# Kernel optimization log

Measured on AMD Instinct MI355X. Metric: run time of the kernel, lower is better.

## Reference

```python
import jax, jax.numpy as jnp
import numpy as np

THETA = 1.0  # integrate-and-fire threshold


def conv2d_t(x, w, b, padding):
    # x: [N,C,H,W,T]; torch snn.conv is Conv3d with kernel (k,k,1) => per-timestep 2D conv
    N, C, H, W, T = x.shape
    xt = jnp.moveaxis(x, -1, 1).reshape(N * T, C, H, W)
    y = jax.lax.conv_general_dilated(
        xt, w, (1, 1), [(padding, padding), (padding, padding)],
        dimension_numbers=('NCHW', 'OIHW', 'NCHW'))
    y = y + b[None, :, None, None]
    O, Ho, Wo = y.shape[1:]
    return jnp.moveaxis(y.reshape(N, T, O, Ho, Wo), 1, -1)


def avg_pool2_t(x):
    # snn.pool(2): fixed-weight 2x2 conv == 2x2 average pool, applied per timestep
    N, C, H, W, T = x.shape
    return x.reshape(N, C, H // 2, 2, W // 2, 2, T).mean(axis=(3, 5))


def dense_t(x, w, b):
    # snn.dense: Conv3d over full spatial extent == linear over flattened C*H*W, per timestep
    N = x.shape[0]; T = x.shape[-1]
    xf = x.reshape(N, -1, T)  # flatten in (C,H,W) order, matching torch conv3d weight layout
    return jnp.einsum('nft,of->not', xf, w) + b[None, :, None]


def spike(x):
    # Temporal LIF (integrate-and-fire, soft reset) scanned over trailing time dim.
    def step(u, xt):
        u = u + xt
        s = (u >= THETA).astype(x.dtype)
        u = u - s * THETA
        return u, s
    xt = jnp.moveaxis(x, -1, 0)  # [T, ...]
    _, s = jax.lax.scan(step, jnp.zeros(x.shape[:-1], x.dtype), xt)
    return jnp.moveaxis(s, 0, -1)


def setup_inputs() -> dict:
    key = jax.random.key(0)
    ks = jax.random.split(key, 20)
    f32 = jnp.float32
    def w(k, shape, fan_in):
        return jax.random.normal(k, shape, f32) * np.float32(1.0 / np.sqrt(fan_in))
    inp = {
        'x':  jax.random.uniform(ks[0], (128, 1, 28, 28, 16), f32),
        'w1': w(ks[1], (32, 1, 3, 3), 9),      'b1': jnp.zeros((32,), f32),
        'w2': w(ks[2], (32, 32, 3, 3), 288),   'b2': jnp.zeros((32,), f32),
        'w3': w(ks[3], (32, 32, 3, 3), 288),   'b3': jnp.zeros((32,), f32),
        'w4': w(ks[4], (16, 32, 1, 1), 32),    'b4': jnp.zeros((16,), f32),
        'w5': w(ks[5], (16, 16, 3, 3), 144),   'b5': jnp.zeros((16,), f32),
        'w6': w(ks[6], (32, 16, 1, 1), 16),    'b6': jnp.zeros((32,), f32),
        'wf1': w(ks[7], (128, 32 * 14 * 14), 32 * 14 * 14), 'bf1': jnp.zeros((128,), f32),
        'wf2': w(ks[8], (10, 128), 128),       'bf2': jnp.zeros((10,), f32),
    }
    return inp


def reference(x, w1, b1, w2, b2, w3, b3, w4, b4, w5, b5, w6, b6, wf1, bf1, wf2, bf2):
    T = x.shape[-1]
    h = spike(conv2d_t(x, w1, b1, 1))
    y = h
    h = spike(conv2d_t(h, w2, b2, 1))
    h = spike(conv2d_t(h, w3, b3, 1) + y)
    h = spike(avg_pool2_t(h))
    y1 = h
    h = spike(conv2d_t(h, w4, b4, 0))
    h = spike(conv2d_t(h, w5, b5, 1))
    h = spike(conv2d_t(h, w6, b6, 0) + y1)
    h = spike(dense_t(h, wf1, bf1))
    h = spike(dense_t(h, wf2, bf2))
    return h.sum(axis=-1) / T  # [N, 10] firing rates
```

## Files before the change

kernel.cpp:

```cpp
#include <hip/hip_runtime.h>

typedef unsigned short u16;
typedef unsigned int u32;
typedef unsigned long long u64;
typedef __attribute__((ext_vector_type(4))) int i32x4;
typedef __attribute__((ext_vector_type(16))) int i32x16;

#define TT 16
#define Z16 {0, 0, 0, 0, 0, 0, 0, 0, 0, 0, 0, 0, 0, 0, 0, 0}

__device__ __forceinline__ u32 scan_spike(const double* acc) {
  double u = 0.0;
  u32 m = 0;
#pragma unroll
  for (int t = 0; t < TT; ++t) {
    u += acc[t];
    if (u >= 1.0) { m |= (1u << t); u -= 1.0; }
  }
  return m;
}

__device__ __forceinline__ long long shfl_xor64(long long v, int m) {
  int lo = __shfl_xor((int)(v & 0xffffffffLL), m);
  int hi = __shfl_xor((int)(v >> 32), m);
  return ((long long)hi << 32) | (u32)lo;
}

__device__ __forceinline__ float conv1_fetch(const float* __restrict__ xn,
                                             int y0, int r, int col, int t) {
  int yi = y0 - 1 + r, xi = col - 1;
  if ((unsigned)yi < 28u && (unsigned)xi < 28u)
    return xn[((size_t)(yi * 28 + xi)) * 16 + t];
  return 0.0f;
}

__global__ __launch_bounds__(448) void conv1_lds(
    const float* __restrict__ x, const float* __restrict__ w,
    const float* __restrict__ b, u16* __restrict__ out) {
  __shared__ float xt[2][4][30][20];
  __shared__ float wl[32][9];

  int blk = blockIdx.x;
  int n = blk >> 1;
  int half = blk & 1;
  int ypBase = half * 7;
  int tid = threadIdx.x;

  for (int i = tid; i < 288; i += 448) wl[i / 9][i % 9] = w[i];

  int sr_[5], sc_[5], st_[5];
  bool sok[5];
#pragma unroll
  for (int k = 0; k < 5; ++k) {
    int i = tid + k * 448;
    sok[k] = (i < 1920);
    int ii = sok[k] ? i : 0;
    sr_[k] = ii / 480;
    int rem = ii % 480;
    sc_[k] = rem / 16;
    st_[k] = rem % 16;
  }
  const float* xn = x + (size_t)n * (28 * 28 * 16);

  int ocg = tid & 7;
  int xx = (tid >> 3) % 28;
  int dy = tid / 224;
  int oc0 = ocg * 4;

  {
    int y0 = ypBase * 2;
#pragma unroll
    for (int k = 0; k < 5; ++k)
      if (sok[k])
        xt[0][sr_[k]][sc_[k]][st_[k]] =
            conv1_fetch(xn, y0, sr_[k], sc_[k], st_[k]);
  }
  __syncthreads();

  float wr[4][9];
#pragma unroll
  for (int j = 0; j < 4; ++j)
#pragma unroll
    for (int ko = 0; ko < 9; ++ko) wr[j][ko] = wl[oc0 + j][ko];
  float bf[4];
#pragma unroll
  for (int j = 0; j < 4; ++j) bf[j] = b[oc0 + j];

  for (int it = 0; it < 7; ++it) {
    int y0 = (ypBase + it) * 2;
    int cur = it & 1;

    float pf[5];
    if (it < 6) {
      int y0n = y0 + 2;
#pragma unroll
      for (int k = 0; k < 5; ++k)
        pf[k] = sok[k] ? conv1_fetch(xn, y0n, sr_[k], sc_[k], st_[k]) : 0.0f;
    }

    double u[4] = {0.0, 0.0, 0.0, 0.0};
    u32 m[4] = {0u, 0u, 0u, 0u};

    const float* row0 = &xt[cur][dy + 0][xx][0];
    const float* row1 = &xt[cur][dy + 1][xx][0];
    const float* row2 = &xt[cur][dy + 2][xx][0];

#pragma unroll
    for (int q = 0; q < 4; ++q) {
      float4 xq[9];
#pragma unroll
      for (int kx = 0; kx < 3; ++kx) {
        xq[0 * 3 + kx] = *(const float4*)(row0 + kx * 20 + q * 4);
        xq[1 * 3 + kx] = *(const float4*)(row1 + kx * 20 + q * 4);
        xq[2 * 3 + kx] = *(const float4*)(row2 + kx * 20 + q * 4);
      }
#pragma unroll
      for (int j = 0; j < 4; ++j) {
        float4 s = {0.0f, 0.0f, 0.0f, 0.0f};
#pragma unroll
        for (int ko = 0; ko < 9; ++ko) {
          s.x = fmaf(wr[j][ko], xq[ko].x, s.x);
          s.y = fmaf(wr[j][ko], xq[ko].y, s.y);
          s.z = fmaf(wr[j][ko], xq[ko].z, s.z);
          s.w = fmaf(wr[j][ko], xq[ko].w, s.w);
        }
        float y0f = s.x + bf[j], y1f = s.y + bf[j];
        float y2f = s.z + bf[j], y3f = s.w + bf[j];
        u[j] += (double)y0f;
        if (u[j] >= 1.0) { m[j] |= 1u << (4 * q + 0); u[j] -= 1.0; }
        u[j] += (double)y1f;
        if (u[j] >= 1.0) { m[j] |= 1u << (4 * q + 1); u[j] -= 1.0; }
        u[j] += (double)y2f;
        if (u[j] >= 1.0) { m[j] |= 1u << (4 * q + 2); u[j] -= 1.0; }
        u[j] += (double)y3f;
        if (u[j] >= 1.0) { m[j] |= 1u << (4 * q + 3); u[j] -= 1.0; }
      }
    }

    int yo = y0 + dy;
    u64 pk = (u64)(u16)m[0] | ((u64)(u16)m[1] << 16) |
             ((u64)(u16)m[2] << 32) | ((u64)(u16)m[3] << 48);
    *(u64*)(out + ((size_t)(n * 28 + yo) * 28 + xx) * 32 + oc0) = pk;

    if (it < 6) {
      int nb = (it + 1) & 1;
#pragma unroll
      for (int k = 0; k < 5; ++k)
        if (sok[k]) xt[nb][sr_[k]][sc_[k]][st_[k]] = pf[k];
      __syncthreads();
    }
  }
}

__global__ void prep_digits_frag2(const float* __restrict__ wa,
                                  const float* __restrict__ wb,
                                  signed char* __restrict__ Wda,
                                  signed char* __restrict__ Wdb) {
  int bid = blockIdx.x;
  const float* w = (bid < 9) ? wa : wb;
  signed char* Wd = (bid < 9) ? Wda : Wdb;
  int tap = bid % 9;
  int lane = threadIdx.x;
  int oc = lane & 31, kh = lane >> 5;
  for (int j = 0; j < 16; ++j) {
    int c = kh * 16 + j;
    double xv = ldexp((double)w[((size_t)(oc * 32 + c)) * 9 + tap], 29);
    long long X = (long long)rint(xv);
    for (int p = 0; p < 4; ++p) {
      int d = (int)((X + 128) & 255) - 128;
      Wd[((size_t)((p * 9 + tap) * 64 + lane)) * 16 + j] = (signed char)d;
      X = (X - (long long)d) >> 8;
    }
  }
}

__global__ void prep_digits5c(const float* __restrict__ w,
                              signed char* __restrict__ Wd) {
  int tap = blockIdx.x;
  int lane = threadIdx.x;
  int oc = lane & 31, kh = lane >> 5;
  for (int j = 0; j < 16; ++j) {
    long long X = 0;
    if (oc < 16 && kh == 0) {
      double xv = ldexp((double)w[((size_t)(oc * 16 + j)) * 9 + tap], 29);
      X = (long long)rint(xv);
    }
    for (int p = 0; p < 4; ++p) {
      int d = (int)((X + 128) & 255) - 128;
      Wd[((size_t)((p * 9 + tap) * 64 + lane)) * 16 + j] = (signed char)d;
      X = (X - (long long)d) >> 8;
    }
  }
}

__global__ __launch_bounds__(256) void zero_borders(
    signed char* __restrict__ T1, signed char* __restrict__ T2) {
  const int PER = 128 * 116 * 32;
  int idx = blockIdx.x * 256 + threadIdx.x;
  int buf = idx >= PER;
  int r = buf ? idx - PER : idx;
  if (r >= PER) return;
  int c16 = r & 31;
  int site = (r >> 5) % 116;
  int nloc = (r >> 5) / 116;
  int y, x;
  if (site < 30) { y = 0; x = site; }
  else if (site < 60) { y = 29; x = site - 30; }
  else if (site < 88) { x = 0; y = site - 60 + 1; }
  else { x = 29; y = site - 88 + 1; }
  signed char* T = buf ? T2 : T1;
  *(i32x4*)(T + (((size_t)nloc * 30 + y) * 30 + x) * 512 + c16 * 16) =
      (i32x4){0, 0, 0, 0};
}

__global__ __launch_bounds__(256) void expand_masks(
    const u16* __restrict__ s, signed char* __restrict__ T) {
  int site = blockIdx.x * 8 + (threadIdx.x >> 5);
  int gl = threadIdx.x & 31;
  int x = site % 28; int t1 = site / 28;
  int y = t1 % 28;   int nloc = t1 / 28;

  u32 v = (u32)s[(((size_t)nloc * 28 + y) * 28 + x) * 32 + gl];
  const u32 MK[5] = {0x0000FFFFu, 0x00FF00FFu, 0x0F0F0F0Fu,
                     0x33333333u, 0x55555555u};
#pragma unroll
  for (int i = 0; i < 5; ++i) {
    int sh = 16 >> i;
    u32 mk = MK[i];
    u32 p = (u32)__shfl_xor((int)v, sh);
    v = ((gl & sh) == 0) ? ((v & mk) | ((p & mk) << sh))
                         : ((v & ~mk) | ((p & ~mk) >> sh));
  }
  if (gl < 16) {
    u32 dw[8];
#pragma unroll
    for (int d = 0; d < 8; ++d) {
      u32 nib = (v >> (4 * d)) & 0xFu;
      dw[d] = (nib * 0x00204081u) & 0x01010101u;
    }
    signed char* Tp =
        T + (((size_t)nloc * 30 + y + 1) * 30 + (x + 1)) * 512 + gl * 32;
    *(i32x4*)Tp = (i32x4){(int)dw[0], (int)dw[1], (int)dw[2], (int)dw[3]};
    *(i32x4*)(Tp + 16) = (i32x4){(int)dw[4], (int)dw[5], (int)dw[6], (int)dw[7]};
  }
}

__global__ __launch_bounds__(256) void expand_t5c(
    const u16* __restrict__ s, signed char* __restrict__ T) {
  int site = blockIdx.x * 8 + (threadIdx.x >> 5);
  int gl = threadIdx.x & 31;
  int x = site % 14; int t1 = site / 14;
  int y = t1 % 14;   int n = t1 / 14;

  u32 v = 0;
  if (gl < 16) v = (u32)s[(((size_t)n * 16 + gl) * 14 + y) * 14 + x];
  const u32 MK[5] = {0x0000FFFFu, 0x00FF00FFu, 0x0F0F0F0Fu,
                     0x33333333u, 0x55555555u};
#pragma unroll
  for (int i = 0; i < 5; ++i) {
    int sh = 16 >> i;
    u32 mk = MK[i];
    u32 p = (u32)__shfl_xor((int)v, sh);
    v = ((gl & sh) == 0) ? ((v & mk) | ((p & mk) << sh))
                         : ((v & ~mk) | ((p & ~mk) >> sh));
  }
  if (gl < 16) {
    u32 dw[4];
#pragma unroll
    for (int d = 0; d < 4; ++d) {
      u32 nib = (v >> (4 * d)) & 0xFu;
      dw[d] = (nib * 0x00204081u) & 0x01010101u;
    }
    signed char* Tp =
        T + ((((size_t)n * 16 + y + 1) * 16 + (x + 1))) * 512 + gl * 32;
    *(i32x4*)Tp = (i32x4){(int)dw[0], (int)dw[1], (int)dw[2], (int)dw[3]};
    *(i32x4*)(Tp + 16) = (i32x4){0, 0, 0, 0};
  }
}

template <int H, int W, int PADW, int COUT, bool WRITE_T, bool HAS_RES>
__device__ __forceinline__ void epi_i8(long long (&cc)[16], int h, int oc,
                                       int px_out, int y, int nloc, int n_g,
                                       const float* bias,
                                       const u16* __restrict__ res,
                                       signed char* __restrict__ Tout,
                                       u16* __restrict__ mout) {
  long long recv[8];
#pragma unroll
  for (int j = 0; j < 8; ++j) {
    long long send = h ? cc[j] : cc[8 + j];
    recv[j] = shfl_xor64(send, 32);
  }
  long long B29 = 0;
  if (oc < COUT) B29 = (long long)rint((double)bias[oc] * 536870912.0);
  u32 rm = 0;
  if (HAS_RES && px_out < W)
    rm = res[(((size_t)n_g * H + y) * W + px_out) * COUT + oc];
  long long u = 0;
  u32 mo = 0;
  const long long TH = 1LL << 29;
#pragma unroll
  for (int t = 0; t < TT; ++t) {
    int lo = (t & 3) + 4 * (t >> 3);
    int sel = (t >> 2) & 1;
    long long own = h ? cc[8 + lo] : cc[lo];
    long long ut = (sel ^ h) ? recv[lo] : own;
    ut += B29 + (((rm >> t) & 1u) ? TH : 0);
    u += ut;
    if (u >= TH) { mo |= (1u << t); u -= TH; }
  }
  if (px_out < W && oc < COUT) {
    if (WRITE_T) {
      signed char* Tp =
          Tout + (((size_t)nloc * PADW + y + 1) * PADW + px_out + 1) * 512 + oc;
#pragma unroll
      for (int t = 0; t < TT; ++t)
        Tp[t * 32] = (signed char)((mo >> t) & 1u);
    } else {
      mout[(((size_t)n_g * COUT + oc) * H + y) * W + px_out] = (u16)mo;
    }
  }
}

template <int H, int W, int PADW, int COUT, bool WRITE_T, bool HAS_RES>
__global__ __launch_bounds__(256, 2) void conv_i8(
    const signed char* __restrict__ Tin, const signed char* __restrict__ Wd,
    const float* __restrict__ bias, const u16* __restrict__ res,
    signed char* __restrict__ Tout, u16* __restrict__ mout, int nbase) {
  constexpr int TILESX = (W + 15) / 16;
  __shared__ signed char WL[4 * 9 * 1024];
  int tid = threadIdx.x;
  for (int j = tid; j < 2304; j += 256)
    ((i32x4*)WL)[j] = ((const i32x4*)Wd)[j];
  __syncthreads();

  int blk = blockIdx.x;
  int xblk = blk % TILESX; int b2 = blk / TILESX;
  int y = b2 % H;          int nloc = b2 / H;
  int lane = tid & 63, wid = tid >> 6;
  int h = lane >> 5, rowlane = lane & 31;
  int pxr = rowlane >> 4, tA = rowlane & 15;
  int pxb = xblk * 16 + wid * 4;

  i32x4 A0[9], A1[9];
  const signed char* Tn = Tin + (size_t)nloc * (PADW * PADW * 512);
#pragma unroll
  for (int ky = 0; ky < 3; ++ky)
#pragma unroll
    for (int kx = 0; kx < 3; ++kx) {
      int tap = ky * 3 + kx;
      int ypad = y + ky;
      int x0 = pxb + pxr + kx;     if (x0 > PADW - 1) x0 = PADW - 1;
      int x1 = pxb + 2 + pxr + kx; if (x1 > PADW - 1) x1 = PADW - 1;
      A0[tap] = *(const i32x4*)(Tn + ((size_t)(ypad * PADW + x0)) * 512 +
                                tA * 32 + h * 16);
      A1[tap] = *(const i32x4*)(Tn + ((size_t)(ypad * PADW + x1)) * 512 +
                                tA * 32 + h * 16);
    }

  i32x16 cp0[2], cp1[2];
#pragma unroll
  for (int pp = 0; pp < 2; ++pp) {
    i32x16 a0lo = Z16, a0hi = Z16, a1lo = Z16, a1hi = Z16;
#pragma unroll
    for (int tap = 0; tap < 9; ++tap) {
      i32x4 Blo =
          *(const i32x4*)&WL[((size_t)(((2 * pp) * 9 + tap) * 64 + lane)) * 16];
      i32x4 Bhi = *(const i32x4*)&WL[((size_t)(((2 * pp + 1) * 9 + tap) * 64 +
                                               lane)) * 16];
      a0lo = __builtin_amdgcn_mfma_i32_32x32x32_i8(A0[tap], Blo, a0lo, 0, 0, 0);
      a0hi = __builtin_amdgcn_mfma_i32_32x32x32_i8(A0[tap], Bhi, a0hi, 0, 0, 0);
      a1lo = __builtin_amdgcn_mfma_i32_32x32x32_i8(A1[tap], Blo, a1lo, 0, 0, 0);
      a1hi = __builtin_amdgcn_mfma_i32_32x32x32_i8(A1[tap], Bhi, a1hi, 0, 0, 0);
    }
#pragma unroll
    for (int r = 0; r < 16; ++r) {
      cp0[pp][r] = a0lo[r] + (a0hi[r] << 8);
      cp1[pp][r] = a1lo[r] + (a1hi[r] << 8);
    }
  }

  long long c0[16], c1[16];
#pragma unroll
  for (int r = 0; r < 16; ++r) {
    c0[r] = (long long)cp0[0][r] + ((long long)cp0[1][r] << 16);
    c1[r] = (long long)cp1[0][r] + ((long long)cp1[1][r] << 16);
  }

  int n_g = nbase + nloc;
  int oc = rowlane;
  epi_i8<H, W, PADW, COUT, WRITE_T, HAS_RES>(c0, h, oc, pxb + h, y, nloc, n_g,
                                             bias, res, Tout, mout);
  epi_i8<H, W, PADW, COUT, WRITE_T, HAS_RES>(c1, h, oc, pxb + 2 + h, y, nloc,
                                             n_g, bias, res, Tout, mout);
}

__global__ __launch_bounds__(256) void pool_spike(
    const u16* __restrict__ in, u16* __restrict__ out) {
  int idx = blockIdx.x * 256 + threadIdx.x;
  const int total = 128 * 32 * 14 * 14;
  if (idx >= total) return;
  int xx = idx % 14; int t1 = idx / 14;
  int yy = t1 % 14;  int t2 = t1 / 14;
  int c  = t2 % 32;  int n  = t2 / 32;

  const u16* base = in + ((size_t)(n * 32 + c) * 28 + yy * 2) * 28 + xx * 2;
  u32 m00 = base[0], m01 = base[1], m10 = base[28], m11 = base[29];

  u32 q = 0, mo = 0;
#pragma unroll
  for (int t = 0; t < TT; ++t) {
    q += ((m00 >> t) & 1u) + ((m01 >> t) & 1u) + ((m10 >> t) & 1u) +
         ((m11 >> t) & 1u);
    if (q >= 4u) { mo |= (1u << t); q -= 4u; }
  }
  out[idx] = (u16)mo;
}

template <int CIN>
__global__ __launch_bounds__(256) void conv1x1_spike(
    const u16* __restrict__ in, const float* __restrict__ w,
    const float* __restrict__ b, const u16* __restrict__ res,
    u16* __restrict__ out, int N, int Cout, int HW) {
  int idx = blockIdx.x * 256 + threadIdx.x;
  int total = N * Cout * HW;
  if (idx >= total) return;
  int p = idx % HW; int t1 = idx / HW;
  int o = t1 % Cout; int n = t1 / Cout;

  float acc[TT];
  float bv = b[o];
#pragma unroll
  for (int t = 0; t < TT; ++t) acc[t] = bv;

  const u16* inp = in + (size_t)n * CIN * HW + p;
  const float* wo = w + (size_t)o * CIN;
#pragma unroll 4
  for (int c = 0; c < CIN; ++c) {
    u32 m = inp[c * HW];
    float wh = 0.5f * wo[c];
#pragma unroll
    for (int t = 0; t < TT; ++t) {
      u32 hi = (m << (30 - t)) & 0x40000000u;
      acc[t] = fmaf(wh, __uint_as_float(hi), acc[t]);
    }
  }
  if (res) {
    u32 m = res[idx];
#pragma unroll
    for (int t = 0; t < TT; ++t) acc[t] += ((m >> t) & 1u) ? 1.0f : 0.0f;
  }
  double u = 0.0;
  u32 mo = 0;
#pragma unroll
  for (int t = 0; t < TT; ++t) {
    u += (double)acc[t];
    if (u >= 1.0) { mo |= (1u << t); u -= 1.0; }
  }
  out[idx] = (u16)mo;
}

__global__ __launch_bounds__(256) void expand_t7(
    const u16* __restrict__ s, signed char* __restrict__ T) {
  int site = blockIdx.x * 8 + (threadIdx.x >> 5);
  int gl = threadIdx.x & 31;
  int fc = site % 196; int n = site / 196;

  u32 v = (u32)s[(size_t)n * 6272 + fc * 32 + gl];
  const u32 MK[5] = {0x0000FFFFu, 0x00FF00FFu, 0x0F0F0F0Fu,
                     0x33333333u, 0x55555555u};
#pragma unroll
  for (int i = 0; i < 5; ++i) {
    int sh = 16 >> i;
    u32 mk = MK[i];
    u32 p = (u32)__shfl_xor((int)v, sh);
    v = ((gl & sh) == 0) ? ((v & mk) | ((p & mk) << sh))
                         : ((v & ~mk) | ((p & ~mk) >> sh));
  }
  if (gl < 16) {
    u32 dw[8];
#pragma unroll
    for (int d = 0; d < 8; ++d) {
      u32 nib = (v >> (4 * d)) & 0xFu;
      dw[d] = (nib * 0x00204081u) & 0x01010101u;
    }
    signed char* Tp = T + ((size_t)n * 16 + gl) * 6272 + fc * 32;
    *(i32x4*)Tp = (i32x4){(int)dw[0], (int)dw[1], (int)dw[2], (int)dw[3]};
    *(i32x4*)(Tp + 16) = (i32x4){(int)dw[4], (int)dw[5], (int)dw[6], (int)dw[7]};
  }
}

__global__ __launch_bounds__(256) void prep_dense_digits(
    const float* __restrict__ w, signed char* __restrict__ Wd) {
  int linear = blockIdx.x * 256 + threadIdx.x;
  int lane = linear & 63;
  int kc = (linear >> 6) % 196;
  int pg = (linear >> 6) / 196;
  int p = pg % 6, g = pg / 6;
  int col = lane & 31, kh = lane >> 5;
  int o = g * 32 + col, fb = kc * 32 + kh * 16;

  alignas(16) signed char dig[16];
#pragma unroll
  for (int j = 0; j < 16; ++j) {
    double xv = (double)w[(size_t)o * 6272 + fb + j] * 35184372088832.0;
    long long X = (long long)rint(xv);
    unsigned long long Y = (unsigned long long)(X + 0x808080808080LL);
    dig[j] = (signed char)(int)(((Y >> (8 * p)) & 255u) - 128);
  }
  *(i32x4*)(Wd + (size_t)linear * 16) = *(const i32x4*)dig;
}

__global__ __launch_bounds__(256) void dense1_part(
    const signed char* __restrict__ T7, const signed char* __restrict__ Wd,
    long long* __restrict__ Pbuf) {
  __shared__ long long red[3][64][16];
  int tid = threadIdx.x, lane = tid & 63, wid = tid >> 6;
  int bidx = blockIdx.x;
  int Mt = bidx & 63;
  int g = (bidx >> 6) & 3;
  int ks = bidx >> 8;
  int n0 = Mt * 2;
  int nl = (lane >> 4) & 1, tA = lane & 15, kh = lane >> 5;

  const signed char* Arow =
      T7 + ((size_t)(n0 + nl) * 16 + tA) * 6272 + kh * 16;
  const signed char* Bbase = Wd + (size_t)g * 6 * 196 * 1024 + lane * 16;

  int slot = ks * 4 + wid;
  int kc0 = slot * 12 + (slot < 4 ? slot : 4);
  int len = (slot < 4) ? 13 : 12;

  i32x16 acc[6];
#pragma unroll
  for (int p = 0; p < 6; ++p)
#pragma unroll
    for (int r = 0; r < 16; ++r) acc[p][r] = 0;

  for (int kc = kc0; kc < kc0 + len; ++kc) {
    i32x4 Af = *(const i32x4*)(Arow + (size_t)kc * 32);
#pragma unroll
    for (int p = 0; p < 6; ++p) {
      i32x4 Bf = *(const i32x4*)(Bbase + (size_t)(p * 196 + kc) * 1024);
      acc[p] = __builtin_amdgcn_mfma_i32_32x32x32_i8(Af, Bf, acc[p], 0, 0, 0);
    }
  }

  long long cc[16];
#pragma unroll
  for (int r = 0; r < 16; ++r) {
    long long v = 0;
#pragma unroll
    for (int p = 0; p < 6; ++p) v += ((long long)acc[p][r]) << (8 * p);
    cc[r] = v;
  }

  if (wid) {
#pragma unroll
    for (int r = 0; r < 16; ++r) red[wid - 1][lane][r] = cc[r];
  }
  __syncthreads();
  if (wid == 0) {
#pragma unroll
    for (int w2 = 0; w2 < 3; ++w2)
#pragma unroll
      for (int r = 0; r < 16; ++r) cc[r] += red[w2][lane][r];
    long long* P = Pbuf + ((size_t)(ks * 256 + Mt * 4 + g)) * 1024 + lane * 16;
#pragma unroll
    for (int r = 0; r < 16; ++r) P[r] = cc[r];
  }
}

__global__ __launch_bounds__(64) void dense1_scan(
    const long long* __restrict__ Pbuf, const float* __restrict__ bias,
    u16* __restrict__ out) {
  int bidx = blockIdx.x;
  int lane = threadIdx.x;
  int g = bidx & 3, n0 = (bidx >> 2) * 2;

  long long cc[16];
#pragma unroll
  for (int r = 0; r < 16; ++r) cc[r] = 0;
#pragma unroll
  for (int ks = 0; ks < 4; ++ks) {
    const long long* P =
        Pbuf + ((size_t)(ks * 256 + bidx)) * 1024 + lane * 16;
#pragma unroll
    for (int r = 0; r < 16; ++r) cc[r] += P[r];
  }

  int h = lane >> 5, col = lane & 31;
  long long recv[8];
#pragma unroll
  for (int j = 0; j < 8; ++j) {
    long long send = h ? cc[j] : cc[8 + j];
    recv[j] = shfl_xor64(send, 32);
  }
  long long B45 =
      (long long)rint((double)bias[g * 32 + col] * 35184372088832.0);
  long long u = 0;
  u32 mo = 0;
  const long long TH = 1LL << 45;
#pragma unroll
  for (int t = 0; t < TT; ++t) {
    int lo = (t & 3) + 4 * (t >> 3);
    int sel = (t >> 2) & 1;
    long long own = h ? cc[8 + lo] : cc[lo];
    long long ut = (sel ^ h) ? recv[lo] : own;
    ut += B45;
    u += ut;
    if (u >= TH) { mo |= (1u << t); u -= TH; }
  }
  out[(n0 + h) * 128 + g * 32 + col] = (u16)mo;
}

__global__ __launch_bounds__(64) void dense2_out(
    const u16* __restrict__ in, const float* __restrict__ w,
    const float* __restrict__ b, float* __restrict__ out) {
  int idx = blockIdx.x * 64 + threadIdx.x;
  if (idx >= 1280) return;
  int o = idx % 10;
  int n = idx / 10;

  double acc[TT];
  double bv = (double)b[o];
#pragma unroll
  for (int t = 0; t < TT; ++t) acc[t] = bv;

  const u16* inn = in + (size_t)n * 128;
  const float* wo = w + (size_t)o * 128;
  for (int f = 0; f < 128; ++f) {
    u32 m = inn[f];
    double wv = (double)wo[f];
#pragma unroll
    for (int t = 0; t < TT; ++t) acc[t] += ((m >> t) & 1u) ? wv : 0.0;
  }
  u32 mo = scan_spike(acc);
  out[idx] = (float)__popc(mo) * 0.0625f;
}

extern "C" void kernel_launch(void* const* d_in, const int* in_sizes, int n_in,
                              void* d_out, int out_size, void* d_ws,
                              size_t ws_size, hipStream_t stream) {
  const float* x   = (const float*)d_in[0];
  const float* w1  = (const float*)d_in[1];
  const float* b1  = (const float*)d_in[2];
  const float* w2  = (const float*)d_in[3];
  const float* b2  = (const float*)d_in[4];
  const float* w3  = (const float*)d_in[5];
  const float* b3  = (const float*)d_in[6];
  const float* w4  = (const float*)d_in[7];
  const float* b4  = (const float*)d_in[8];
  const float* w5  = (const float*)d_in[9];
  const float* b5  = (const float*)d_in[10];
  const float* w6  = (const float*)d_in[11];
  const float* b6  = (const float*)d_in[12];
  const float* wf1 = (const float*)d_in[13];
  const float* bf1 = (const float*)d_in[14];
  const float* wf2 = (const float*)d_in[15];
  const float* bf2 = (const float*)d_in[16];
  float* out = (float*)d_out;

  char* W = (char*)d_ws;
  u16* s1 = (u16*)(W + 0);
  u16* s3 = (u16*)(W + 6422528);
  u16* s4 = (u16*)(W + 12845056);
  u16* s5 = (u16*)(W + 14450688);
  u16* s6 = (u16*)(W + 15253504);
  u16* s7 = (u16*)(W + 16056320);
  u16* s8 = (u16*)(W + 17661952);
  signed char* Wd2 = (signed char*)(W + 17694720);
  signed char* Wd3 = (signed char*)(W + 17750016);
  signed char* T1f = (signed char*)(W + 17805312);
  signed char* T2f = (signed char*)(W + 76787712);
  signed char* T5c  = T1f;
  signed char* Wd5c = (signed char*)(W + 34582528);
  signed char* Wd1 = T2f;
  long long*  Pbuf = (long long*)((char*)T2f + 5242880);
  signed char* T7  = T1f;

  prep_digits_frag2<<<18, 64, 0, stream>>>(w2, w3, Wd2, Wd3);
  zero_borders<<<3712, 256, 0, stream>>>(T1f, T2f);

  conv1_lds<<<256, 448, 0, stream>>>(x, w1, b1, s1);

  expand_masks<<<12544, 256, 0, stream>>>(s1, T1f);
  conv_i8<28, 28, 30, 32, true, false><<<7168, 256, 0, stream>>>(
      T1f, Wd2, b2, nullptr, T2f, nullptr, 0);
  conv_i8<28, 28, 30, 32, false, true><<<7168, 256, 0, stream>>>(
      T2f, Wd3, b3, s1, nullptr, s3, 0);

  pool_spike<<<3136, 256, 0, stream>>>(s3, s4);
  conv1x1_spike<32><<<1568, 256, 0, stream>>>(s4, w4, b4, nullptr, s5, 128, 16,
                                              196);
  hipMemsetAsync(T5c, 0, 16777216, stream);
  prep_digits5c<<<9, 64, 0, stream>>>(w5, Wd5c);
  expand_t5c<<<3136, 256, 0, stream>>>(s5, T5c);
  conv_i8<14, 14, 16, 16, false, false><<<1792, 256, 0, stream>>>(
      T5c, Wd5c, b5, nullptr, nullptr, s6, 0);
  conv1x1_spike<16><<<3136, 256, 0, stream>>>(s6, w6, b6, s4, s7, 128, 32, 196);

  expand_t7<<<3136, 256, 0, stream>>>(s7, T7);
  prep_dense_digits<<<1176, 256, 0, stream>>>(wf1, Wd1);
  dense1_part<<<1024, 256, 0, stream>>>(T7, Wd1, Pbuf);
  dense1_scan<<<256, 64, 0, stream>>>(Pbuf, bf1, s8);

  dense2_out<<<20, 64, 0, stream>>>(s8, wf2, bf2, out);
}
```

Measured before the change: 502.2 us.

## Split conv_i8 pixel pairs across two waves with 512-thread blocks

Each wave in conv_i8 now computes one pixel-pair tile, where before it computed two. Blocks double to 512 threads so the same 16-pixel row segment is still covered. This roughly halves per-wave registers for A fragments and accumulators, which may allow more waves in flight, and amortizes the LDS weight load over more waves. In exchange each wave reuses each B fragment loaded from LDS half as often, so LDS reads per MFMA rise.

New measurement: 464.5 us. 1.08x faster.

```diff
diff --git a/kernel.cpp b/kernel.cpp
--- a/kernel.cpp
+++ b/kernel.cpp
@@ -323,14 +323,14 @@
 }
 
 template <int H, int W, int PADW, int COUT, bool WRITE_T, bool HAS_RES>
-__global__ __launch_bounds__(256, 2) void conv_i8(
+__global__ __launch_bounds__(512, 2) void conv_i8(
     const signed char* __restrict__ Tin, const signed char* __restrict__ Wd,
     const float* __restrict__ bias, const u16* __restrict__ res,
     signed char* __restrict__ Tout, u16* __restrict__ mout, int nbase) {
   constexpr int TILESX = (W + 15) / 16;
   __shared__ signed char WL[4 * 9 * 1024];
   int tid = threadIdx.x;
-  for (int j = tid; j < 2304; j += 256)
+  for (int j = tid; j < 2304; j += 512)
     ((i32x4*)WL)[j] = ((const i32x4*)Wd)[j];
   __syncthreads();
 
@@ -340,9 +340,10 @@
   int lane = tid & 63, wid = tid >> 6;
   int h = lane >> 5, rowlane = lane & 31;
   int pxr = rowlane >> 4, tA = rowlane & 15;
-  int pxb = xblk * 16 + wid * 4;
-
-  i32x4 A0[9], A1[9];
+  int wtile = wid >> 1, sel = wid & 1;
+  int pxb = xblk * 16 + wtile * 4 + sel * 2;
+
+  i32x4 A[9];
   const signed char* Tn = Tin + (size_t)nloc * (PADW * PADW * 512);
 #pragma unroll
   for (int ky = 0; ky < 3; ++ky)
@@ -350,49 +351,38 @@
     for (int kx = 0; kx < 3; ++kx) {
       int tap = ky * 3 + kx;
       int ypad = y + ky;
-      int x0 = pxb + pxr + kx;     if (x0 > PADW - 1) x0 = PADW - 1;
-      int x1 = pxb + 2 + pxr + kx; if (x1 > PADW - 1) x1 = PADW - 1;
-      A0[tap] = *(const i32x4*)(Tn + ((size_t)(ypad * PADW + x0)) * 512 +
-                                tA * 32 + h * 16);
-      A1[tap] = *(const i32x4*)(Tn + ((size_t)(ypad * PADW + x1)) * 512 +
-                                tA * 32 + h * 16);
-    }
-
-  i32x16 cp0[2], cp1[2];
+      int x0 = pxb + pxr + kx;
+      if (x0 > PADW - 1) x0 = PADW - 1;
+      A[tap] = *(const i32x4*)(Tn + ((size_t)(ypad * PADW + x0)) * 512 +
+                               tA * 32 + h * 16);
+    }
+
+  i32x16 cp[2];
 #pragma unroll
   for (int pp = 0; pp < 2; ++pp) {
-    i32x16 a0lo = Z16, a0hi = Z16, a1lo = Z16, a1hi = Z16;
+    i32x16 alo = Z16, ahi = Z16;
 #pragma unroll
     for (int tap = 0; tap < 9; ++tap) {
       i32x4 Blo =
           *(const i32x4*)&WL[((size_t)(((2 * pp) * 9 + tap) * 64 + lane)) * 16];
       i32x4 Bhi = *(const i32x4*)&WL[((size_t)(((2 * pp + 1) * 9 + tap) * 64 +
                                                lane)) * 16];
-      a0lo = __builtin_amdgcn_mfma_i32_32x32x32_i8(A0[tap], Blo, a0lo, 0, 0, 0);
-      a0hi = __builtin_amdgcn_mfma_i32_32x32x32_i8(A0[tap], Bhi, a0hi, 0, 0, 0);
-      a1lo = __builtin_amdgcn_mfma_i32_32x32x32_i8(A1[tap], Blo, a1lo, 0, 0, 0);
-      a1hi = __builtin_amdgcn_mfma_i32_32x32x32_i8(A1[tap], Bhi, a1hi, 0, 0, 0);
-    }
-#pragma unroll
-    for (int r = 0; r < 16; ++r) {
-      cp0[pp][r] = a0lo[r] + (a0hi[r] << 8);
-      cp1[pp][r] = a1lo[r] + (a1hi[r] << 8);
-    }
-  }
-
-  long long c0[16], c1[16];
-#pragma unroll
-  for (int r = 0; r < 16; ++r) {
-    c0[r] = (long long)cp0[0][r] + ((long long)cp0[1][r] << 16);
-    c1[r] = (long long)cp1[0][r] + ((long long)cp1[1][r] << 16);
-  }
+      alo = __builtin_amdgcn_mfma_i32_32x32x32_i8(A[tap], Blo, alo, 0, 0, 0);
+      ahi = __builtin_amdgcn_mfma_i32_32x32x32_i8(A[tap], Bhi, ahi, 0, 0, 0);
+    }
+#pragma unroll
+    for (int r = 0; r < 16; ++r) cp[pp][r] = alo[r] + (ahi[r] << 8);
+  }
+
+  long long c0[16];
+#pragma unroll
+  for (int r = 0; r < 16; ++r)
+    c0[r] = (long long)cp[0][r] + ((long long)cp[1][r] << 16);
 
   int n_g = nbase + nloc;
   int oc = rowlane;
   epi_i8<H, W, PADW, COUT, WRITE_T, HAS_RES>(c0, h, oc, pxb + h, y, nloc, n_g,
                                              bias, res, Tout, mout);
-  epi_i8<H, W, PADW, COUT, WRITE_T, HAS_RES>(c1, h, oc, pxb + 2 + h, y, nloc,
-                                             n_g, bias, res, Tout, mout);
 }
 
 __global__ __launch_bounds__(256) void pool_spike(
@@ -685,9 +675,9 @@
   conv1_lds<<<256, 448, 0, stream>>>(x, w1, b1, s1);
 
   expand_masks<<<12544, 256, 0, stream>>>(s1, T1f);
-  conv_i8<28, 28, 30, 32, true, false><<<7168, 256, 0, stream>>>(
+  conv_i8<28, 28, 30, 32, true, false><<<7168, 512, 0, stream>>>(
       T1f, Wd2, b2, nullptr, T2f, nullptr, 0);
-  conv_i8<28, 28, 30, 32, false, true><<<7168, 256, 0, stream>>>(
+  conv_i8<28, 28, 30, 32, false, true><<<7168, 512, 0, stream>>>(
       T2f, Wd3, b3, s1, nullptr, s3, 0);
 
   pool_spike<<<3136, 256, 0, stream>>>(s3, s4);
@@ -696,7 +686,7 @@
   hipMemsetAsync(T5c, 0, 16777216, stream);
   prep_digits5c<<<9, 64, 0, stream>>>(w5, Wd5c);
   expand_t5c<<<3136, 256, 0, stream>>>(s5, T5c);
-  conv_i8<14, 14, 16, 16, false, false><<<1792, 256, 0, stream>>>(
+  conv_i8<14, 14, 16, 16, false, false><<<1792, 512, 0, stream>>>(
       T5c, Wd5c, b5, nullptr, nullptr, s6, 0);
   conv1x1_spike<16><<<3136, 256, 0, stream>>>(s6, w6, b6, s4, s7, 128, 32, 196);
 
```
